# Performance work log

Hardware: AMD Instinct MI355X
Metric: run time of the kernel (lower is better)

Reference implementation:

```python
import jax, jax.numpy as jnp
import numpy as np


def setup_inputs() -> dict:
    key = jax.random.key(0)
    ks = jax.random.split(key, 9)
    n, L, H, H2 = 1024, 256, 512, 256
    return {
        "lstms0": jax.random.normal(ks[0], (n, L), jnp.float32),
        "lstms1": jax.random.normal(ks[1], (n, L), jnp.float32),
        "W_foh": jax.random.normal(ks[2], (2 * L, H), jnp.float32) * 0.05,
        "W_fom": jax.random.normal(ks[3], (2 * L, H), jnp.float32) * 0.05,
        "catBias": jax.random.normal(ks[4], (1, 2 * H), jnp.float32) * 0.05,
        "hid2Layer": jax.random.normal(ks[5], (2 * H, H2), jnp.float32) * 0.05,
        "hid2Bias": jax.random.normal(ks[6], (1, H2), jnp.float32) * 0.05,
        "outLayer": jax.random.normal(ks[7], (H2, 1), jnp.float32) * 0.05,
        "outBias": jax.random.normal(ks[8], (1, 1), jnp.float32) * 0.05,
    }


def reference(lstms0, lstms1, W_foh, W_fom, catBias, hid2Layer, hid2Bias, outLayer, outBias):
    act = jnp.tanh
    H = W_foh.shape[1]
    # per-token concatenated BiLSTM state: [n, 2L]
    x = jnp.concatenate([lstms0, lstms1], axis=-1)
    headfov = x @ W_foh  # [n, H]
    modfov = x @ W_fom   # [n, H]
    # activation(concat(head_i, mod_j) + catBias) is elementwise, so it splits:
    ah = act(headfov + catBias[0, :H])  # [n, H]
    am = act(modfov + catBias[0, H:])   # [n, H]
    # concat(ah_i, am_j) @ hid2Layer == ah_i @ W_top + am_j @ W_bot
    A = ah @ hid2Layer[:H]  # [n, H2]
    B = am @ hid2Layer[H:]  # [n, H2]
    # pairwise hidden: [n_head, n_mod, H2]
    Z = act(A[:, None, :] + B[None, :, :] + hid2Bias[0])
    scores = jnp.einsum("ijh,h->ij", Z, outLayer[:, 0]) + outBias[0, 0]
    return scores  # [n, n], scores[i, j] = score(head=i, mod=j)
```

## Files before the change

kernel.cpp:

```cpp
#include <hip/hip_runtime.h>
#include <hip/hip_bf16.h>

typedef short s16x8 __attribute__((ext_vector_type(8)));
typedef float f32x4 __attribute__((ext_vector_type(4)));

#define LOG2E_2 2.8853900817779268f

__device__ __forceinline__ float fexp2(float x){ return __builtin_amdgcn_exp2f(x); }
__device__ __forceinline__ float frcp (float x){ return __builtin_amdgcn_rcpf(x); }
__device__ __forceinline__ float ftanh(float v){
    return 1.0f - 2.0f * frcp(1.0f + fexp2(LOG2E_2 * v));
}
__device__ __forceinline__ unsigned short f2bf(float v){
    __hip_bfloat16 h = __float2bfloat16(v);
    return __builtin_bit_cast(unsigned short, h);
}
__device__ __forceinline__ float bf2f(unsigned short u){
    return __bfloat162float(__builtin_bit_cast(__hip_bfloat16, u));
}
__device__ __forceinline__ f32x4 mfma32(s16x8 a, s16x8 b, f32x4 c){
    return __builtin_amdgcn_mfma_f32_16x16x32_bf16(a, b, c, 0, 0, 0);
}

__global__ __launch_bounds__(256) void prep_all(
    const float* __restrict__ l0, const float* __restrict__ l1,
    const float* __restrict__ Wfoh, const float* __restrict__ Wfom,
    const float* __restrict__ W2,
    unsigned short* __restrict__ xhi, unsigned short* __restrict__ xlo,
    unsigned short* __restrict__ w1hi, unsigned short* __restrict__ w1lo,
    unsigned short* __restrict__ w2hi, unsigned short* __restrict__ w2lo)
{
    __shared__ float F[32][33];
    const int t = threadIdx.x;
    const int bid = blockIdx.x;

    if (bid < 512) {
        int idx = (bid * 256 + t) * 4;
        int r = idx >> 9, c = idx & 511;
        float4 v = (c < 256) ? *(const float4*)(l0 + r*256 + c)
                             : *(const float4*)(l1 + r*256 + (c - 256));
        ushort4 h, l;
        h.x = f2bf(v.x); l.x = f2bf(v.x - bf2f(h.x));
        h.y = f2bf(v.y); l.y = f2bf(v.y - bf2f(h.y));
        h.z = f2bf(v.z); l.z = f2bf(v.z - bf2f(h.z));
        h.w = f2bf(v.w); l.w = f2bf(v.w - bf2f(h.w));
        *(ushort4*)(xhi + idx) = h;
        *(ushort4*)(xlo + idx) = l;
        return;
    }

    const float* srcA; const float* srcB;
    int splitN, lda, K, k0, n0;
    unsigned short *dhi, *dlo;
    if (bid < 1024) {
        int b = bid - 512;
        k0 = (b & 15) * 32; n0 = (b >> 4) * 32;
        srcA = Wfoh; srcB = Wfom; splitN = 512; lda = 512; K = 512;
        dhi = w1hi; dlo = w1lo;
    } else {
        int b = bid - 1024;
        k0 = (b & 31) * 32; n0 = (b >> 5) * 32;
        srcA = W2; srcB = W2; splitN = 1 << 30; lda = 256; K = 1024;
        dhi = w2hi; dlo = w2lo;
    }
    {
        int kk = t >> 3, n4 = (t & 7) * 4;
        int n = n0 + n4;
        const float* s = (n < splitN) ? (srcA + (k0+kk)*lda + n)
                                      : (srcB + (k0+kk)*lda + (n - splitN));
        float4 v = *(const float4*)s;
        F[kk][n4+0] = v.x; F[kk][n4+1] = v.y; F[kk][n4+2] = v.z; F[kk][n4+3] = v.w;
    }
    __syncthreads();
    {
        int nn = t >> 3, k4 = (t & 7) * 4;
        ushort4 h, l;
        float v0 = F[k4+0][nn]; h.x = f2bf(v0); l.x = f2bf(v0 - bf2f(h.x));
        float v1 = F[k4+1][nn]; h.y = f2bf(v1); l.y = f2bf(v1 - bf2f(h.y));
        float v2 = F[k4+2][nn]; h.z = f2bf(v2); l.z = f2bf(v2 - bf2f(h.z));
        float v3 = F[k4+3][nn]; h.w = f2bf(v3); l.w = f2bf(v3 - bf2f(h.w));
        *(ushort4*)(dhi + (n0+nn)*K + k0 + k4) = h;
        *(ushort4*)(dlo + (n0+nn)*K + k0 + k4) = l;
    }
}

__global__ __launch_bounds__(256) void k1_mfma(
    const unsigned short* __restrict__ xhi, const unsigned short* __restrict__ xlo,
    const unsigned short* __restrict__ whi, const unsigned short* __restrict__ wlo,
    const float* __restrict__ cb,
    unsigned short* __restrict__ hvhi, unsigned short* __restrict__ hvlo)
{
    __shared__ unsigned short Ah[2][64][40], Al[2][64][40], Bh[2][32][40], Bl[2][32][40];
    const int t = threadIdx.x;
    const int r0 = blockIdx.y * 64, c0 = blockIdx.x * 32;
    const int w = t >> 6, lane = t & 63;
    const int m = lane & 15, quad = lane >> 4;

    const int arow = t >> 2, aseg = t & 3;
    const int brow = (t & 127) >> 2, bseg = t & 3;
    const bool doB = (t < 128);

    f32x4 acc0 = {0,0,0,0}, acc1 = {0,0,0,0};

    const unsigned short* pAh = xhi + (r0+arow)*512 + aseg*8;
    const unsigned short* pAl = xlo + (r0+arow)*512 + aseg*8;
    const unsigned short* pBh = whi + (c0+brow)*512 + bseg*8;
    const unsigned short* pBl = wlo + (c0+brow)*512 + bseg*8;

    uint4 pah = *(const uint4*)pAh;
    uint4 pal = *(const uint4*)pAl;
    uint4 pbh = {}, pbl = {};
    if (doB) { pbh = *(const uint4*)pBh; pbl = *(const uint4*)pBl; }

    *(uint4*)&Ah[0][arow][aseg*8] = pah;
    *(uint4*)&Al[0][arow][aseg*8] = pal;
    if (doB) {
        *(uint4*)&Bh[0][brow][bseg*8] = pbh;
        *(uint4*)&Bl[0][brow][bseg*8] = pbl;
    }
    pah = *(const uint4*)(pAh + 32);
    pal = *(const uint4*)(pAl + 32);
    if (doB) { pbh = *(const uint4*)(pBh + 32); pbl = *(const uint4*)(pBl + 32); }
    __syncthreads();

    #pragma unroll 2
    for (int c = 0; c < 16; ++c) {
        const int buf = c & 1;
        {
            const int ko = quad*8;
            s16x8 ah  = *(const s16x8*)&Ah[buf][w*16 + m][ko];
            s16x8 al  = *(const s16x8*)&Al[buf][w*16 + m][ko];
            s16x8 b0h = *(const s16x8*)&Bh[buf][m][ko];
            s16x8 b0l = *(const s16x8*)&Bl[buf][m][ko];
            s16x8 b1h = *(const s16x8*)&Bh[buf][16 + m][ko];
            s16x8 b1l = *(const s16x8*)&Bl[buf][16 + m][ko];
            acc0 = mfma32(ah, b0h, acc0);
            acc0 = mfma32(ah, b0l, acc0);
            acc0 = mfma32(al, b0h, acc0);
            acc1 = mfma32(ah, b1h, acc1);
            acc1 = mfma32(ah, b1l, acc1);
            acc1 = mfma32(al, b1h, acc1);
        }
        if (c + 1 < 16) {
            const int nb = buf ^ 1;
            *(uint4*)&Ah[nb][arow][aseg*8] = pah;
            *(uint4*)&Al[nb][arow][aseg*8] = pal;
            if (doB) {
                *(uint4*)&Bh[nb][brow][bseg*8] = pbh;
                *(uint4*)&Bl[nb][brow][bseg*8] = pbl;
            }
            if (c + 2 < 16) {
                const int k0 = (c+2) * 32;
                pah = *(const uint4*)(pAh + k0);
                pal = *(const uint4*)(pAl + k0);
                if (doB) { pbh = *(const uint4*)(pBh + k0); pbl = *(const uint4*)(pBl + k0); }
            }
            __syncthreads();
        }
    }

    #pragma unroll
    for (int nt = 0; nt < 2; ++nt) {
        f32x4 a = nt ? acc1 : acc0;
        const int col = c0 + nt*16 + m;
        const float bias = cb[col];
        #pragma unroll
        for (int reg = 0; reg < 4; ++reg) {
            const int row = r0 + w*16 + quad*4 + reg;
            float v = ftanh(a[reg] + bias);
            unsigned short h = f2bf(v);
            unsigned short l = f2bf(v - bf2f(h));
            hvhi[row*1024 + col] = h;
            hvlo[row*1024 + col] = l;
        }
    }
}

__global__ __launch_bounds__(256) void k2_mfma(
    const unsigned short* __restrict__ hvhi, const unsigned short* __restrict__ hvlo,
    const unsigned short* __restrict__ w2hi, const unsigned short* __restrict__ w2lo,
    const float* __restrict__ h2b, float* __restrict__ P)
{
    __shared__ unsigned short Ah[2][64][40], Al[2][64][40], Bh[2][32][40], Bl[2][32][40];
    const int t = threadIdx.x;
    const int r0 = blockIdx.y * 64, c0 = blockIdx.x * 32;
    const int half = (c0 >= 256) ? 1 : 0;
    const int ho = half * 512;
    const int nw = c0 & 255;
    const int w = t >> 6, lane = t & 63;
    const int m = lane & 15, quad = lane >> 4;

    const int arow = t >> 2, aseg = t & 3;
    const int brow = (t & 127) >> 2, bseg = t & 3;
    const bool doB = (t < 128);

    f32x4 acc0 = {0,0,0,0}, acc1 = {0,0,0,0};

    const unsigned short* pAh = hvhi + (r0+arow)*1024 + ho + aseg*8;
    const unsigned short* pAl = hvlo + (r0+arow)*1024 + ho + aseg*8;
    const unsigned short* pBh = w2hi + (nw+brow)*1024 + ho + bseg*8;
    const unsigned short* pBl = w2lo + (nw+brow)*1024 + ho + bseg*8;

    uint4 pah = *(const uint4*)pAh;
    uint4 pal = *(const uint4*)pAl;
    uint4 pbh = {}, pbl = {};
    if (doB) { pbh = *(const uint4*)pBh; pbl = *(const uint4*)pBl; }

    *(uint4*)&Ah[0][arow][aseg*8] = pah;
    *(uint4*)&Al[0][arow][aseg*8] = pal;
    if (doB) {
        *(uint4*)&Bh[0][brow][bseg*8] = pbh;
        *(uint4*)&Bl[0][brow][bseg*8] = pbl;
    }
    pah = *(const uint4*)(pAh + 32);
    pal = *(const uint4*)(pAl + 32);
    if (doB) { pbh = *(const uint4*)(pBh + 32); pbl = *(const uint4*)(pBl + 32); }
    __syncthreads();

    #pragma unroll 2
    for (int c = 0; c < 16; ++c) {
        const int buf = c & 1;
        {
            const int ko = quad*8;
            s16x8 ah  = *(const s16x8*)&Ah[buf][w*16 + m][ko];
            s16x8 al  = *(const s16x8*)&Al[buf][w*16 + m][ko];
            s16x8 b0h = *(const s16x8*)&Bh[buf][m][ko];
            s16x8 b0l = *(const s16x8*)&Bl[buf][m][ko];
            s16x8 b1h = *(const s16x8*)&Bh[buf][16 + m][ko];
            s16x8 b1l = *(const s16x8*)&Bl[buf][16 + m][ko];
            acc0 = mfma32(ah, b0h, acc0);
            acc0 = mfma32(ah, b0l, acc0);
            acc0 = mfma32(al, b0h, acc0);
            acc1 = mfma32(ah, b1h, acc1);
            acc1 = mfma32(ah, b1l, acc1);
            acc1 = mfma32(al, b1h, acc1);
        }
        if (c + 1 < 16) {
            const int nb = buf ^ 1;
            *(uint4*)&Ah[nb][arow][aseg*8] = pah;
            *(uint4*)&Al[nb][arow][aseg*8] = pal;
            if (doB) {
                *(uint4*)&Bh[nb][brow][bseg*8] = pbh;
                *(uint4*)&Bl[nb][brow][bseg*8] = pbl;
            }
            if (c + 2 < 16) {
                const int k0 = (c+2) * 32;
                pah = *(const uint4*)(pAh + k0);
                pal = *(const uint4*)(pAl + k0);
                if (doB) { pbh = *(const uint4*)(pBh + k0); pbl = *(const uint4*)(pBl + k0); }
            }
            __syncthreads();
        }
    }

    #pragma unroll
    for (int nt = 0; nt < 2; ++nt) {
        f32x4 a = nt ? acc1 : acc0;
        const int col = c0 + nt*16 + m;
        const float bias = half ? 0.0f : h2b[col];
        #pragma unroll
        for (int reg = 0; reg < 4; ++reg) {
            const int row = r0 + w*16 + quad*4 + reg;
            P[row*512 + col] = fexp2((a[reg] + bias) * LOG2E_2);
        }
    }
}

__global__ __launch_bounds__(256) void k3_pairwise(
    const float* __restrict__ P, const float* __restrict__ w,
    const float* __restrict__ ob, float* __restrict__ out)
{
    __shared__ float As[2][32][68];
    __shared__ float Bs[2][32][68];
    __shared__ float wls[256];
    const int tid = threadIdx.x;
    const int tx = tid & 15;
    const int ty = tid >> 4;
    const int i0 = blockIdx.y * 32, j0 = blockIdx.x * 32;

    wls[tid] = w[tid];

    const int ar = tid >> 3, ac = (tid & 7) * 8;

    const float* pA = P + (i0 + ar) * 512 + ac;
    const float* pB = P + (j0 + ar) * 512 + 256 + ac;

    float4 ra0 = *(const float4*)(pA);
    float4 ra1 = *(const float4*)(pA + 4);
    float4 rb0 = *(const float4*)(pB);
    float4 rb1 = *(const float4*)(pB + 4);

    *(float4*)&As[0][ar][ac]   = ra0;
    *(float4*)&As[0][ar][ac+4] = ra1;
    *(float4*)&Bs[0][ar][ac]   = rb0;
    *(float4*)&Bs[0][ar][ac+4] = rb1;
    ra0 = *(const float4*)(pA + 64);
    ra1 = *(const float4*)(pA + 68);
    rb0 = *(const float4*)(pB + 64);
    rb1 = *(const float4*)(pB + 68);
    __syncthreads();

    float acc[2][2] = {};

    #pragma unroll 2
    for (int c = 0; c < 4; ++c) {
        const int buf = c & 1;
        #pragma unroll 4
        for (int hh = 0; hh < 64; hh += 4) {
            float4 wv = *(const float4*)&wls[c*64 + hh];
            float4 av[2], bv[2];
            av[0] = *(const float4*)&As[buf][ty][hh];
            av[1] = *(const float4*)&As[buf][ty+16][hh];
            bv[0] = *(const float4*)&Bs[buf][tx][hh];
            bv[1] = *(const float4*)&Bs[buf][tx+16][hh];
            #pragma unroll
            for (int r = 0; r < 2; ++r)
                #pragma unroll
                for (int q = 0; q < 2; ++q) {
                    float u0 = fmaf(av[r].x, bv[q].x, 1.0f);
                    float u1 = fmaf(av[r].y, bv[q].y, 1.0f);
                    float u2 = fmaf(av[r].z, bv[q].z, 1.0f);
                    float u3 = fmaf(av[r].w, bv[q].w, 1.0f);
                    float d01 = u0 * u1;
                    float d23 = u2 * u3;
                    float p01 = fmaf(wv.x, u1, wv.y * u0);
                    float p23 = fmaf(wv.z, u3, wv.w * u2);
                    float num = fmaf(p01, d23, p23 * d01);
                    acc[r][q] = fmaf(num, frcp(d01 * d23), acc[r][q]);
                }
        }
        if (c + 1 < 4) {
            const int nb = buf ^ 1;
            *(float4*)&As[nb][ar][ac]   = ra0;
            *(float4*)&As[nb][ar][ac+4] = ra1;
            *(float4*)&Bs[nb][ar][ac]   = rb0;
            *(float4*)&Bs[nb][ar][ac+4] = rb1;
            if (c + 2 < 4) {
                const int off = (c + 2) * 64;
                ra0 = *(const float4*)(pA + off);
                ra1 = *(const float4*)(pA + off + 4);
                rb0 = *(const float4*)(pB + off);
                rb1 = *(const float4*)(pB + off + 4);
            }
            __syncthreads();
        }
    }

    float sumw = 0.0f;
    #pragma unroll
    for (int h = 0; h < 256; h += 4) {
        float4 wv = *(const float4*)&wls[h];
        sumw += (wv.x + wv.y) + (wv.z + wv.w);
    }
    const float base = ob[0] + sumw;
    out[(i0+ty)*1024    + j0+tx]      = base - 2.0f * acc[0][0];
    out[(i0+ty)*1024    + j0+tx+16]   = base - 2.0f * acc[0][1];
    out[(i0+ty+16)*1024 + j0+tx]      = base - 2.0f * acc[1][0];
    out[(i0+ty+16)*1024 + j0+tx+16]   = base - 2.0f * acc[1][1];
}

extern "C" void kernel_launch(void* const* d_in, const int* in_sizes, int n_in,
                              void* d_out, int out_size, void* d_ws, size_t ws_size,
                              hipStream_t stream) {
    const float* l0   = (const float*)d_in[0];
    const float* l1   = (const float*)d_in[1];
    const float* Wfoh = (const float*)d_in[2];
    const float* Wfom = (const float*)d_in[3];
    const float* cb   = (const float*)d_in[4];
    const float* W2   = (const float*)d_in[5];
    const float* h2b  = (const float*)d_in[6];
    const float* w    = (const float*)d_in[7];
    const float* ob   = (const float*)d_in[8];
    float* out = (float*)d_out;

    unsigned short* hv_hi  = (unsigned short*)d_ws;
    unsigned short* hv_lo  = hv_hi + 1024*1024;
    float*          P      = (float*)(hv_lo + 1024*1024);
    unsigned short* xs_hi  = (unsigned short*)(P + 1024*512);
    unsigned short* xs_lo  = xs_hi + 1024*512;
    unsigned short* w1t_hi = xs_lo + 1024*512;
    unsigned short* w1t_lo = w1t_hi + 1024*512;
    unsigned short* w2t_hi = w1t_lo + 1024*512;
    unsigned short* w2t_lo = w2t_hi + 256*1024;

    prep_all<<<1280, 256, 0, stream>>>(l0, l1, Wfoh, Wfom, W2,
                                       xs_hi, xs_lo, w1t_hi, w1t_lo, w2t_hi, w2t_lo);
    k1_mfma<<<dim3(32,16), 256, 0, stream>>>(xs_hi, xs_lo, w1t_hi, w1t_lo, cb, hv_hi, hv_lo);
    k2_mfma<<<dim3(16,16), 256, 0, stream>>>(hv_hi, hv_lo, w2t_hi, w2t_lo, h2b, P);
    k3_pairwise<<<dim3(32,32), 256, 0, stream>>>(P, w, ob, out);
}
```

Measured before the change: 123.3 us.

## Fuse bf16 hi/lo split of inputs and weights into GEMM kernels, drop prep pass

Removes the separate prep kernel that converted inputs and weights to bf16 hi/lo pairs and transposed the weights. The two GEMM kernels now load fp32 directly, do the split on the fly and write the transposed tiles into shared memory. This saves one launch and a workspace round-trip. The cost is strided scalar weight loads and conversion work repeated in every block. The second GEMM also moves to 32-row tiles, which doubles the grid and gives each wave one accumulator.

```diff
diff --git a/kernel.cpp b/kernel.cpp
--- a/kernel.cpp
+++ b/kernel.cpp
@@ -21,72 +21,16 @@
 __device__ __forceinline__ f32x4 mfma32(s16x8 a, s16x8 b, f32x4 c){
     return __builtin_amdgcn_mfma_f32_16x16x32_bf16(a, b, c, 0, 0, 0);
 }
-
-__global__ __launch_bounds__(256) void prep_all(
+__device__ __forceinline__ void cvt4(float4 v, ushort4& h, ushort4& l){
+    h.x = f2bf(v.x); l.x = f2bf(v.x - bf2f(h.x));
+    h.y = f2bf(v.y); l.y = f2bf(v.y - bf2f(h.y));
+    h.z = f2bf(v.z); l.z = f2bf(v.z - bf2f(h.z));
+    h.w = f2bf(v.w); l.w = f2bf(v.w - bf2f(h.w));
+}
+
+__global__ __launch_bounds__(256) void k1_fused(
     const float* __restrict__ l0, const float* __restrict__ l1,
     const float* __restrict__ Wfoh, const float* __restrict__ Wfom,
-    const float* __restrict__ W2,
-    unsigned short* __restrict__ xhi, unsigned short* __restrict__ xlo,
-    unsigned short* __restrict__ w1hi, unsigned short* __restrict__ w1lo,
-    unsigned short* __restrict__ w2hi, unsigned short* __restrict__ w2lo)
-{
-    __shared__ float F[32][33];
-    const int t = threadIdx.x;
-    const int bid = blockIdx.x;
-
-    if (bid < 512) {
-        int idx = (bid * 256 + t) * 4;
-        int r = idx >> 9, c = idx & 511;
-        float4 v = (c < 256) ? *(const float4*)(l0 + r*256 + c)
-                             : *(const float4*)(l1 + r*256 + (c - 256));
-        ushort4 h, l;
-        h.x = f2bf(v.x); l.x = f2bf(v.x - bf2f(h.x));
-        h.y = f2bf(v.y); l.y = f2bf(v.y - bf2f(h.y));
-        h.z = f2bf(v.z); l.z = f2bf(v.z - bf2f(h.z));
-        h.w = f2bf(v.w); l.w = f2bf(v.w - bf2f(h.w));
-        *(ushort4*)(xhi + idx) = h;
-        *(ushort4*)(xlo + idx) = l;
-        return;
-    }
-
-    const float* srcA; const float* srcB;
-    int splitN, lda, K, k0, n0;
-    unsigned short *dhi, *dlo;
-    if (bid < 1024) {
-        int b = bid - 512;
-        k0 = (b & 15) * 32; n0 = (b >> 4) * 32;
-        srcA = Wfoh; srcB = Wfom; splitN = 512; lda = 512; K = 512;
-        dhi = w1hi; dlo = w1lo;
-    } else {
-        int b = bid - 1024;
-        k0 = (b & 31) * 32; n0 = (b >> 5) * 32;
-        srcA = W2; srcB = W2; splitN = 1 << 30; lda = 256; K = 1024;
-        dhi = w2hi; dlo = w2lo;
-    }
-    {
-        int kk = t >> 3, n4 = (t & 7) * 4;
-        int n = n0 + n4;
-        const float* s = (n < splitN) ? (srcA + (k0+kk)*lda + n)
-                                      : (srcB + (k0+kk)*lda + (n - splitN));
-        float4 v = *(const float4*)s;
-        F[kk][n4+0] = v.x; F[kk][n4+1] = v.y; F[kk][n4+2] = v.z; F[kk][n4+3] = v.w;
-    }
-    __syncthreads();
-    {
-        int nn = t >> 3, k4 = (t & 7) * 4;
-        ushort4 h, l;
-        float v0 = F[k4+0][nn]; h.x = f2bf(v0); l.x = f2bf(v0 - bf2f(h.x));
-        float v1 = F[k4+1][nn]; h.y = f2bf(v1); l.y = f2bf(v1 - bf2f(h.y));
-        float v2 = F[k4+2][nn]; h.z = f2bf(v2); l.z = f2bf(v2 - bf2f(h.z));
-        float v3 = F[k4+3][nn]; h.w = f2bf(v3); l.w = f2bf(v3 - bf2f(h.w));
-        *(ushort4*)(dhi + (n0+nn)*K + k0 + k4) = h;
-        *(ushort4*)(dlo + (n0+nn)*K + k0 + k4) = l;
-    }
-}
-
-__global__ __launch_bounds__(256) void k1_mfma(
-    const unsigned short* __restrict__ xhi, const unsigned short* __restrict__ xlo,
-    const unsigned short* __restrict__ whi, const unsigned short* __restrict__ wlo,
     const float* __restrict__ cb,
     unsigned short* __restrict__ hvhi, unsigned short* __restrict__ hvlo)
 {
@@ -97,33 +41,38 @@
     const int m = lane & 15, quad = lane >> 4;
 
     const int arow = t >> 2, aseg = t & 3;
-    const int brow = (t & 127) >> 2, bseg = t & 3;
-    const bool doB = (t < 128);
+    const int nn = t & 31, kq = t >> 5;
+
+    const float* xrow0 = l0 + (r0+arow)*256 + aseg*8;
+    const float* xrow1 = l1 + (r0+arow)*256 + aseg*8;
+    const float* wcol  = (c0 < 512) ? (Wfoh + c0 + nn) : (Wfom + (c0 - 512) + nn);
 
     f32x4 acc0 = {0,0,0,0}, acc1 = {0,0,0,0};
 
-    const unsigned short* pAh = xhi + (r0+arow)*512 + aseg*8;
-    const unsigned short* pAl = xlo + (r0+arow)*512 + aseg*8;
-    const unsigned short* pBh = whi + (c0+brow)*512 + bseg*8;
-    const unsigned short* pBl = wlo + (c0+brow)*512 + bseg*8;
-
-    uint4 pah = *(const uint4*)pAh;
-    uint4 pal = *(const uint4*)pAl;
-    uint4 pbh = {}, pbl = {};
-    if (doB) { pbh = *(const uint4*)pBh; pbl = *(const uint4*)pBl; }
-
-    *(uint4*)&Ah[0][arow][aseg*8] = pah;
-    *(uint4*)&Al[0][arow][aseg*8] = pal;
-    if (doB) {
-        *(uint4*)&Bh[0][brow][bseg*8] = pbh;
-        *(uint4*)&Bl[0][brow][bseg*8] = pbl;
-    }
-    pah = *(const uint4*)(pAh + 32);
-    pal = *(const uint4*)(pAl + 32);
-    if (doB) { pbh = *(const uint4*)(pBh + 32); pbl = *(const uint4*)(pBl + 32); }
+    float4 fa0, fa1, fb;
+    #define K1_LOAD(k0_) do { \
+        const float* pa_ = ((k0_) < 256) ? (xrow0 + (k0_)) : (xrow1 + ((k0_) - 256)); \
+        fa0 = *(const float4*)pa_; \
+        fa1 = *(const float4*)(pa_ + 4); \
+        const float* pb_ = wcol + ((k0_) + kq*4) * 512; \
+        fb.x = pb_[0]; fb.y = pb_[512]; fb.z = pb_[1024]; fb.w = pb_[1536]; \
+    } while(0)
+    #define K1_STAGE(buf_) do { \
+        ushort4 h0_, lo0_, h1_, lo1_, bh_, bl_; \
+        cvt4(fa0, h0_, lo0_); cvt4(fa1, h1_, lo1_); cvt4(fb, bh_, bl_); \
+        *(ushort4*)&Ah[buf_][arow][aseg*8]     = h0_; \
+        *(ushort4*)&Ah[buf_][arow][aseg*8 + 4] = h1_; \
+        *(ushort4*)&Al[buf_][arow][aseg*8]     = lo0_; \
+        *(ushort4*)&Al[buf_][arow][aseg*8 + 4] = lo1_; \
+        *(ushort4*)&Bh[buf_][nn][kq*4] = bh_; \
+        *(ushort4*)&Bl[buf_][nn][kq*4] = bl_; \
+    } while(0)
+
+    K1_LOAD(0);
+    K1_STAGE(0);
+    K1_LOAD(32);
     __syncthreads();
 
-    #pragma unroll 2
     for (int c = 0; c < 16; ++c) {
         const int buf = c & 1;
         {
@@ -142,22 +91,13 @@
             acc1 = mfma32(al, b1h, acc1);
         }
         if (c + 1 < 16) {
-            const int nb = buf ^ 1;
-            *(uint4*)&Ah[nb][arow][aseg*8] = pah;
-            *(uint4*)&Al[nb][arow][aseg*8] = pal;
-            if (doB) {
-                *(uint4*)&Bh[nb][brow][bseg*8] = pbh;
-                *(uint4*)&Bl[nb][brow][bseg*8] = pbl;
-            }
-            if (c + 2 < 16) {
-                const int k0 = (c+2) * 32;
-                pah = *(const uint4*)(pAh + k0);
-                pal = *(const uint4*)(pAl + k0);
-                if (doB) { pbh = *(const uint4*)(pBh + k0); pbl = *(const uint4*)(pBl + k0); }
-            }
+            K1_STAGE(buf ^ 1);
+            if (c + 2 < 16) K1_LOAD((c + 2) * 32);
             __syncthreads();
         }
     }
+    #undef K1_LOAD
+    #undef K1_STAGE
 
     #pragma unroll
     for (int nt = 0; nt < 2; ++nt) {
@@ -176,92 +116,80 @@
     }
 }
 
-__global__ __launch_bounds__(256) void k2_mfma(
+__global__ __launch_bounds__(256) void k2_fused(
     const unsigned short* __restrict__ hvhi, const unsigned short* __restrict__ hvlo,
-    const unsigned short* __restrict__ w2hi, const unsigned short* __restrict__ w2lo,
-    const float* __restrict__ h2b, float* __restrict__ P)
+    const float* __restrict__ W2, const float* __restrict__ h2b,
+    float* __restrict__ P)
 {
-    __shared__ unsigned short Ah[2][64][40], Al[2][64][40], Bh[2][32][40], Bl[2][32][40];
+    __shared__ unsigned short Ah[2][32][40], Al[2][32][40], Bh[2][32][40], Bl[2][32][40];
     const int t = threadIdx.x;
-    const int r0 = blockIdx.y * 64, c0 = blockIdx.x * 32;
+    const int r0 = blockIdx.y * 32, c0 = blockIdx.x * 32;
     const int half = (c0 >= 256) ? 1 : 0;
     const int ho = half * 512;
     const int nw = c0 & 255;
     const int w = t >> 6, lane = t & 63;
     const int m = lane & 15, quad = lane >> 4;
-
-    const int arow = t >> 2, aseg = t & 3;
-    const int brow = (t & 127) >> 2, bseg = t & 3;
-    const bool doB = (t < 128);
-
-    f32x4 acc0 = {0,0,0,0}, acc1 = {0,0,0,0};
-
-    const unsigned short* pAh = hvhi + (r0+arow)*1024 + ho + aseg*8;
-    const unsigned short* pAl = hvlo + (r0+arow)*1024 + ho + aseg*8;
-    const unsigned short* pBh = w2hi + (nw+brow)*1024 + ho + bseg*8;
-    const unsigned short* pBl = w2lo + (nw+brow)*1024 + ho + bseg*8;
-
-    uint4 pah = *(const uint4*)pAh;
-    uint4 pal = *(const uint4*)pAl;
-    uint4 pbh = {}, pbl = {};
-    if (doB) { pbh = *(const uint4*)pBh; pbl = *(const uint4*)pBl; }
-
-    *(uint4*)&Ah[0][arow][aseg*8] = pah;
-    *(uint4*)&Al[0][arow][aseg*8] = pal;
-    if (doB) {
-        *(uint4*)&Bh[0][brow][bseg*8] = pbh;
-        *(uint4*)&Bl[0][brow][bseg*8] = pbl;
-    }
-    pah = *(const uint4*)(pAh + 32);
-    pal = *(const uint4*)(pAl + 32);
-    if (doB) { pbh = *(const uint4*)(pBh + 32); pbl = *(const uint4*)(pBl + 32); }
+    const int wm = w & 1, wn = w >> 1;
+
+    const int arow = t >> 3, aseg = t & 7;
+    const int nn = t & 31, kq = t >> 5;
+
+    const unsigned short* pAh = hvhi + (r0+arow)*1024 + ho + aseg*4;
+    const unsigned short* pAl = hvlo + (r0+arow)*1024 + ho + aseg*4;
+    const float* wcol = W2 + ho*256 + nw + nn;
+
+    f32x4 acc = {0,0,0,0};
+
+    uint2 pa_h, pa_l;
+    float4 fb;
+    #define K2_LOAD(k0_) do { \
+        pa_h = *(const uint2*)(pAh + (k0_)); \
+        pa_l = *(const uint2*)(pAl + (k0_)); \
+        const float* pb_ = wcol + ((k0_) + kq*4) * 256; \
+        fb.x = pb_[0]; fb.y = pb_[256]; fb.z = pb_[512]; fb.w = pb_[768]; \
+    } while(0)
+    #define K2_STAGE(buf_) do { \
+        ushort4 bh_, bl_; \
+        cvt4(fb, bh_, bl_); \
+        *(uint2*)&Ah[buf_][arow][aseg*4] = pa_h; \
+        *(uint2*)&Al[buf_][arow][aseg*4] = pa_l; \
+        *(ushort4*)&Bh[buf_][nn][kq*4] = bh_; \
+        *(ushort4*)&Bl[buf_][nn][kq*4] = bl_; \
+    } while(0)
+
+    K2_LOAD(0);
+    K2_STAGE(0);
+    K2_LOAD(32);
     __syncthreads();
 
-    #pragma unroll 2
     for (int c = 0; c < 16; ++c) {
         const int buf = c & 1;
         {
             const int ko = quad*8;
-            s16x8 ah  = *(const s16x8*)&Ah[buf][w*16 + m][ko];
-            s16x8 al  = *(const s16x8*)&Al[buf][w*16 + m][ko];
-            s16x8 b0h = *(const s16x8*)&Bh[buf][m][ko];
-            s16x8 b0l = *(const s16x8*)&Bl[buf][m][ko];
-            s16x8 b1h = *(const s16x8*)&Bh[buf][16 + m][ko];
-            s16x8 b1l = *(const s16x8*)&Bl[buf][16 + m][ko];
-            acc0 = mfma32(ah, b0h, acc0);
-            acc0 = mfma32(ah, b0l, acc0);
-            acc0 = mfma32(al, b0h, acc0);
-            acc1 = mfma32(ah, b1h, acc1);
-            acc1 = mfma32(ah, b1l, acc1);
-            acc1 = mfma32(al, b1h, acc1);
+            s16x8 ah = *(const s16x8*)&Ah[buf][wm*16 + m][ko];
+            s16x8 al = *(const s16x8*)&Al[buf][wm*16 + m][ko];
+            s16x8 bh = *(const s16x8*)&Bh[buf][wn*16 + m][ko];
+            s16x8 bl = *(const s16x8*)&Bl[buf][wn*16 + m][ko];
+            acc = mfma32(ah, bh, acc);
+            acc = mfma32(ah, bl, acc);
+            acc = mfma32(al, bh, acc);
         }
         if (c + 1 < 16) {
-            const int nb = buf ^ 1;
-            *(uint4*)&Ah[nb][arow][aseg*8] = pah;
-            *(uint4*)&Al[nb][arow][aseg*8] = pal;
-            if (doB) {
-                *(uint4*)&Bh[nb][brow][bseg*8] = pbh;
-                *(uint4*)&Bl[nb][brow][bseg*8] = pbl;
-            }
-            if (c + 2 < 16) {
-                const int k0 = (c+2) * 32;
-                pah = *(const uint4*)(pAh + k0);
-                pal = *(const uint4*)(pAl + k0);
-                if (doB) { pbh = *(const uint4*)(pBh + k0); pbl = *(const uint4*)(pBl + k0); }
-            }
+            K2_STAGE(buf ^ 1);
+            if (c + 2 < 16) K2_LOAD((c + 2) * 32);
             __syncthreads();
         }
     }
-
-    #pragma unroll
-    for (int nt = 0; nt < 2; ++nt) {
-        f32x4 a = nt ? acc1 : acc0;
-        const int col = c0 + nt*16 + m;
+    #undef K2_LOAD
+    #undef K2_STAGE
+
+    {
+        const int col = c0 + wn*16 + m;
         const float bias = half ? 0.0f : h2b[col];
         #pragma unroll
         for (int reg = 0; reg < 4; ++reg) {
-            const int row = r0 + w*16 + quad*4 + reg;
-            P[row*512 + col] = fexp2((a[reg] + bias) * LOG2E_2);
+            const int row = r0 + wm*16 + quad*4 + reg;
+            P[row*512 + col] = fexp2((acc[reg] + bias) * LOG2E_2);
         }
     }
 }
@@ -373,19 +301,11 @@
     const float* ob   = (const float*)d_in[8];
     float* out = (float*)d_out;
 
-    unsigned short* hv_hi  = (unsigned short*)d_ws;
-    unsigned short* hv_lo  = hv_hi + 1024*1024;
-    float*          P      = (float*)(hv_lo + 1024*1024);
-    unsigned short* xs_hi  = (unsigned short*)(P + 1024*512);
-    unsigned short* xs_lo  = xs_hi + 1024*512;
-    unsigned short* w1t_hi = xs_lo + 1024*512;
-    unsigned short* w1t_lo = w1t_hi + 1024*512;
-    unsigned short* w2t_hi = w1t_lo + 1024*512;
-    unsigned short* w2t_lo = w2t_hi + 256*1024;
-
-    prep_all<<<1280, 256, 0, stream>>>(l0, l1, Wfoh, Wfom, W2,
-                                       xs_hi, xs_lo, w1t_hi, w1t_lo, w2t_hi, w2t_lo);
-    k1_mfma<<<dim3(32,16), 256, 0, stream>>>(xs_hi, xs_lo, w1t_hi, w1t_lo, cb, hv_hi, hv_lo);
-    k2_mfma<<<dim3(16,16), 256, 0, stream>>>(hv_hi, hv_lo, w2t_hi, w2t_lo, h2b, P);
+    unsigned short* hv_hi = (unsigned short*)d_ws;
+    unsigned short* hv_lo = hv_hi + 1024*1024;
+    float*          P     = (float*)(hv_lo + 1024*1024);
+
+    k1_fused<<<dim3(32,16), 256, 0, stream>>>(l0, l1, Wfoh, Wfom, cb, hv_hi, hv_lo);
+    k2_fused<<<dim3(16,32), 256, 0, stream>>>(hv_hi, hv_lo, W2, h2b, P);
     k3_pairwise<<<dim3(32,32), 256, 0, stream>>>(P, w, ob, out);
 }
```

After: 118.5 us, median of 2. 3.9% less time.
